# Kernel optimization log

Measured on AMD Instinct MI355X. Metric: run time of the kernel, lower is better.

Reference implementation:

```python
import jax, jax.numpy as jnp
import numpy as np
import math

B, S, D, H = 4, 1024, 1024, 16
DK = D // H


def setup_inputs() -> dict:
    key = jax.random.key(0)
    ks = jax.random.split(key, 12)
    inp = {
        "q": jax.random.normal(ks[0], (B, S, D), jnp.float32),
        "k": jax.random.normal(ks[1], (B, S, D), jnp.float32),
        "v": jax.random.normal(ks[2], (B, S, D), jnp.float32),
        # causal mask, broadcast over batch (0 = masked)
        "mask": jnp.broadcast_to(jnp.tril(jnp.ones((S, S), jnp.int32)), (B, S, S)),
    }
    sc = 1.0 / math.sqrt(D)
    # torch nn.Linear convention: y = x @ W.T + b, W:[out,in]
    inp["Wq"] = jax.random.normal(ks[3], (D, D), jnp.float32) * sc
    inp["bq"] = jnp.zeros((D,), jnp.float32)
    inp["Wk"] = jax.random.normal(ks[4], (D, D), jnp.float32) * sc
    inp["bk"] = jnp.zeros((D,), jnp.float32)
    inp["Wv"] = jax.random.normal(ks[5], (D, D), jnp.float32) * sc
    inp["bv"] = jnp.zeros((D,), jnp.float32)
    inp["Wo"] = jax.random.normal(ks[6], (D, D), jnp.float32) * sc
    inp["bo"] = jnp.zeros((D,), jnp.float32)
    return inp


def _mha(q, k, v, mask, Wq, bq, Wk, bk, Wv, bv, Wo, bo):
    def split_heads(x):  # [B,S,D] -> [B,H,S,DK]
        return x.reshape(B, S, H, DK).transpose(0, 2, 1, 3)

    qh = split_heads(q @ Wq.T + bq)
    kh = split_heads(k @ Wk.T + bk)
    vh = split_heads(v @ Wv.T + bv)

    scores = jnp.einsum("bhqd,bhkd->bhqk", qh, kh) / math.sqrt(DK)
    scores = jnp.where(mask[:, None, :, :] == 0, jnp.float32(-1e9), scores)
    weights = jax.nn.softmax(scores, axis=-1)  # dropout in eval mode -> identity
    out = jnp.einsum("bhqk,bhkd->bhqd", weights, vh)
    out = out.transpose(0, 2, 1, 3).reshape(B, S, D)
    return out @ Wo.T + bo


def reference(q, k, v, mask, Wq, bq, Wk, bk, Wv, bv, Wo, bo):
    return _mha(q, k, v, mask, Wq, bq, Wk, bk, Wv, bv, Wo, bo)
```

## Files before the change

### kernel.cpp

```cpp
#include <hip/hip_runtime.h>

typedef unsigned short u16;
typedef __bf16 bf16x8 __attribute__((ext_vector_type(8)));
typedef float floatx4 __attribute__((ext_vector_type(4)));

#define BB 4
#define SS 1024
#define DD 1024
#define HH 16
#define DKK 64
#define MM (BB*SS)

__device__ __forceinline__ u16 f2bf(float f) {
    union { float f; unsigned int u; } v; v.f = f;
    unsigned int r = v.u + 0x7fffu + ((v.u >> 16) & 1u);
    return (u16)(r >> 16);
}

__device__ __forceinline__ void async16(const u16* g, u16* l) {
    __builtin_amdgcn_global_load_lds(
        (const __attribute__((address_space(1))) void*)g,
        (__attribute__((address_space(3))) void*)l,
        16, 0, 0);
}

__global__ __launch_bounds__(256) void convert_kernel(
    const float* __restrict__ q, const float* __restrict__ k, const float* __restrict__ v,
    const float* __restrict__ Wq, const float* __restrict__ Wk, const float* __restrict__ Wv,
    const float* __restrict__ Wo,
    u16* qb, u16* kb, u16* vb, u16* Wqb, u16* Wkb, u16* Wvb, u16* Wob) {
    const int Q4 = (BB*SS*DD) / 4;
    const int W4 = (DD*DD) / 4;
    int idx = blockIdx.x * 256 + threadIdx.x;
    const float* src; u16* dst; int off;
    if (idx < Q4)            { src = q; dst = qb; off = idx; }
    else if (idx < 2*Q4)     { src = k; dst = kb; off = idx - Q4; }
    else if (idx < 3*Q4)     { src = v; dst = vb; off = idx - 2*Q4; }
    else {
        int r = idx - 3*Q4;
        int wsel = r / W4; off = r - wsel*W4;
        src = wsel==0 ? Wq : wsel==1 ? Wk : wsel==2 ? Wv : Wo;
        dst = wsel==0 ? Wqb : wsel==1 ? Wkb : wsel==2 ? Wvb : Wob;
    }
    float4 x = ((const float4*)src)[off];
    ushort4 y;
    y.x = f2bf(x.x); y.y = f2bf(x.y); y.z = f2bf(x.z); y.w = f2bf(x.w);
    ((ushort4*)dst)[off] = y;
}

__global__ __launch_bounds__(256) void qkv_gemm(
    const u16* __restrict__ qb, const u16* __restrict__ kb, const u16* __restrict__ vb,
    const u16* __restrict__ Wqb, const u16* __restrict__ Wkb, const u16* __restrict__ Wvb,
    const float* __restrict__ bq, const float* __restrict__ bk, const float* __restrict__ bv,
    u16* Qh, u16* Kh, u16* Vt) {
    const int K = DD;
    __shared__ u16 sA[128*32];
    __shared__ u16 sW[128*32];
    int nb = blockIdx.x;
    int m0 = blockIdx.y * 128;
    int which = nb >> 3;
    int n0 = (nb & 7) * 128;
    const u16* A   = which==0 ? qb  : which==1 ? kb  : vb;
    const u16* W   = which==0 ? Wqb : which==1 ? Wkb : Wvb;
    const float* bias = which==0 ? bq : which==1 ? bk : bv;
    u16* Out = which==0 ? Qh : which==1 ? Kh : Vt;
    float scale = which==0 ? 0.125f : 1.0f;

    int t = threadIdx.x;
    int w = t >> 6, l = t & 63, g = l >> 4, c = l & 15;
    int wm = w & 1, wn = w >> 1;
    int sw = (g ^ (c & 3)) * 8;

    floatx4 acc[4][4] = {};

    int srow = t >> 2;
    int sseg = (t & 3) ^ (srow & 3);
    const u16* gA0 = A + (size_t)(m0 + srow) * K + sseg*8;
    const u16* gW0 = W + (size_t)(n0 + srow) * K + sseg*8;
    u16* lA = &sA[t*8];
    u16* lW = &sW[t*8];

    for (int kk = 0; kk < K; kk += 32) {
        __syncthreads();
        async16(gA0 + kk,          lA);
        async16(gA0 + 64*K + kk,   lA + 64*32);
        async16(gW0 + kk,          lW);
        async16(gW0 + 64*K + kk,   lW + 64*32);
        __syncthreads();
        bf16x8 af[4], bf_[4];
        #pragma unroll
        for (int i = 0; i < 4; i++) af[i]  = *(const bf16x8*)&sA[(wm*64 + i*16 + c)*32 + sw];
        #pragma unroll
        for (int j = 0; j < 4; j++) bf_[j] = *(const bf16x8*)&sW[(wn*64 + j*16 + c)*32 + sw];
        #pragma unroll
        for (int i = 0; i < 4; i++)
            #pragma unroll
            for (int j = 0; j < 4; j++)
                acc[i][j] = __builtin_amdgcn_mfma_f32_16x16x32_bf16(af[i], bf_[j], acc[i][j], 0, 0, 0);
    }

    #pragma unroll
    for (int j = 0; j < 4; j++) {
        int col = n0 + wn*64 + j*16 + c;
        float bb = bias[col];
        int h = col >> 6, dk = col & 63;
        #pragma unroll
        for (int i = 0; i < 4; i++) {
            #pragma unroll
            for (int r = 0; r < 4; r++) {
                int row = m0 + wm*64 + i*16 + g*4 + r;
                int b = row >> 10, s = row & 1023;
                float vv = (acc[i][j][r] + bb) * scale;
                u16 bits = f2bf(vv);
                if (which == 2) {
                    Out[((size_t)((b*HH + h)*DKK + dk))*SS + s] = bits;
                } else {
                    Out[((size_t)(b*HH + h)*SS + s)*DKK + dk] = bits;
                }
            }
        }
    }
}

__global__ __launch_bounds__(256) void attn_kernel(
    const u16* __restrict__ Qh, const u16* __restrict__ Kh, const u16* __restrict__ Vt,
    u16* __restrict__ attnO) {
    __shared__ u16 sQ[64*72];
    __shared__ u16 sK[64*72];
    __shared__ u16 sVt[64*72];
    __shared__ u16 sP[64*72];

    int bh = blockIdx.y;
    const u16* Qp  = Qh + (size_t)bh * SS * DKK;
    const u16* Kp  = Kh + (size_t)bh * SS * DKK;
    const u16* Vtp = Vt + (size_t)bh * DKK * SS;
    int b = bh >> 4, h = bh & 15;

    int t = threadIdx.x, w = t >> 6, l = t & 63, g = l >> 4, c = l & 15;
    int wq = w * 16;

    #pragma unroll
    for (int phase = 0; phase < 2; phase++) {
        int qt = phase == 0 ? (15 - (int)blockIdx.x) : (int)blockIdx.x;
        int q0 = qt * 64;

        __syncthreads();
        #pragma unroll
        for (int p = 0; p < 2; p++) {
            int seg = t + p*256;
            int row = seg >> 3, sc = seg & 7;
            *(uint4*)&sQ[row*72 + sc*8] = *(const uint4*)&Qp[(q0 + row)*DKK + sc*8];
        }

        float l_[4] = {0.f, 0.f, 0.f, 0.f};
        floatx4 o[4] = {};

        for (int k0 = 0; k0 <= q0; k0 += 64) {
            __syncthreads();
            #pragma unroll
            for (int p = 0; p < 2; p++) {
                int seg = t + p*256;
                int row = seg >> 3, sc = seg & 7;
                *(uint4*)&sK[row*72 + sc*8]  = *(const uint4*)&Kp[(k0 + row)*DKK + sc*8];
                *(uint4*)&sVt[row*72 + sc*8] = *(const uint4*)&Vtp[row*SS + k0 + sc*8];
            }
            __syncthreads();

            floatx4 sc_[4] = {};
            #pragma unroll
            for (int ks = 0; ks < 2; ks++) {
                bf16x8 aq = *(const bf16x8*)&sQ[(wq + c)*72 + ks*32 + g*8];
                #pragma unroll
                for (int nt = 0; nt < 4; nt++) {
                    bf16x8 bk_ = *(const bf16x8*)&sK[(nt*16 + c)*72 + ks*32 + g*8];
                    sc_[nt] = __builtin_amdgcn_mfma_f32_16x16x32_bf16(aq, bk_, sc_[nt], 0, 0, 0);
                }
            }

            if (k0 == q0) {
                #pragma unroll
                for (int nt = 0; nt < 4; nt++)
                    #pragma unroll
                    for (int r = 0; r < 4; r++) {
                        int qg = wq + g*4 + r;
                        int kg = nt*16 + c;
                        if (kg > qg) sc_[nt][r] = -1e30f;
                    }
            }

            #pragma unroll
            for (int r = 0; r < 4; r++) {
                float rs = 0.f;
                #pragma unroll
                for (int nt = 0; nt < 4; nt++) {
                    float p = __expf(sc_[nt][r]);
                    sc_[nt][r] = p;
                    rs += p;
                }
                rs += __shfl_xor(rs, 1);
                rs += __shfl_xor(rs, 2);
                rs += __shfl_xor(rs, 4);
                rs += __shfl_xor(rs, 8);
                l_[r] += rs;
                int prow = (wq + g*4 + r)*72;
                #pragma unroll
                for (int nt = 0; nt < 4; nt++)
                    sP[prow + nt*16 + c] = f2bf(sc_[nt][r]);
            }

            #pragma unroll
            for (int ks = 0; ks < 2; ks++) {
                bf16x8 ap = *(const bf16x8*)&sP[(wq + c)*72 + ks*32 + g*8];
                #pragma unroll
                for (int nt = 0; nt < 4; nt++) {
                    bf16x8 bv_ = *(const bf16x8*)&sVt[(nt*16 + c)*72 + ks*32 + g*8];
                    o[nt] = __builtin_amdgcn_mfma_f32_16x16x32_bf16(ap, bv_, o[nt], 0, 0, 0);
                }
            }
        }

        #pragma unroll
        for (int r = 0; r < 4; r++) {
            float inv = 1.0f / l_[r];
            int row = q0 + wq + g*4 + r;
            #pragma unroll
            for (int nt = 0; nt < 4; nt++) {
                int dcol = h*64 + nt*16 + c;
                attnO[((size_t)b*SS + row)*DD + dcol] = f2bf(o[nt][r] * inv);
            }
        }
    }
}

__global__ __launch_bounds__(256) void out_gemm(
    const u16* __restrict__ A, const u16* __restrict__ W,
    const float* __restrict__ bo, float* __restrict__ out) {
    const int K = DD;
    __shared__ u16 sA[64*32];
    __shared__ u16 sW[128*32];
    int n0 = blockIdx.x * 128;
    int m0 = blockIdx.y * 64;

    int t = threadIdx.x;
    int w = t >> 6, l = t & 63, g = l >> 4, c = l & 15;
    int wm = w & 1, wn = w >> 1;
    int sw = (g ^ (c & 3)) * 8;

    floatx4 acc[2][4] = {};

    int srow = t >> 2;
    int sseg = (t & 3) ^ (srow & 3);
    const u16* gA0 = A + (size_t)(m0 + srow) * K + sseg*8;
    const u16* gW0 = W + (size_t)(n0 + srow) * K + sseg*8;
    u16* lA = &sA[t*8];
    u16* lW = &sW[t*8];

    for (int kk = 0; kk < K; kk += 32) {
        __syncthreads();
        async16(gA0 + kk,        lA);
        async16(gW0 + kk,        lW);
        async16(gW0 + 64*K + kk, lW + 64*32);
        __syncthreads();
        bf16x8 af[2], bf_[4];
        #pragma unroll
        for (int i = 0; i < 2; i++) af[i]  = *(const bf16x8*)&sA[(wm*32 + i*16 + c)*32 + sw];
        #pragma unroll
        for (int j = 0; j < 4; j++) bf_[j] = *(const bf16x8*)&sW[(wn*64 + j*16 + c)*32 + sw];
        #pragma unroll
        for (int i = 0; i < 2; i++)
            #pragma unroll
            for (int j = 0; j < 4; j++)
                acc[i][j] = __builtin_amdgcn_mfma_f32_16x16x32_bf16(af[i], bf_[j], acc[i][j], 0, 0, 0);
    }

    #pragma unroll
    for (int j = 0; j < 4; j++) {
        int col = n0 + wn*64 + j*16 + c;
        float bb = bo[col];
        #pragma unroll
        for (int i = 0; i < 2; i++) {
            #pragma unroll
            for (int r = 0; r < 4; r++) {
                int row = m0 + wm*32 + i*16 + g*4 + r;
                out[(size_t)row*DD + col] = acc[i][j][r] + bb;
            }
        }
    }
}

extern "C" void kernel_launch(void* const* d_in, const int* in_sizes, int n_in,
                              void* d_out, int out_size, void* d_ws, size_t ws_size,
                              hipStream_t stream) {
    const float* q    = (const float*)d_in[0];
    const float* k    = (const float*)d_in[1];
    const float* v    = (const float*)d_in[2];
    const float* Wq   = (const float*)d_in[4];
    const float* bq   = (const float*)d_in[5];
    const float* Wk   = (const float*)d_in[6];
    const float* bk   = (const float*)d_in[7];
    const float* Wv   = (const float*)d_in[8];
    const float* bv   = (const float*)d_in[9];
    const float* Wo   = (const float*)d_in[10];
    const float* bo   = (const float*)d_in[11];
    float* out = (float*)d_out;

    char* ws = (char*)d_ws;
    const size_t MB = 1024*1024;
    u16* qb   = (u16*)(ws + 0*MB);
    u16* kb   = (u16*)(ws + 8*MB);
    u16* vb   = (u16*)(ws + 16*MB);
    u16* Wqb  = (u16*)(ws + 24*MB);
    u16* Wkb  = (u16*)(ws + 26*MB);
    u16* Wvb  = (u16*)(ws + 28*MB);
    u16* Wob  = (u16*)(ws + 30*MB);
    u16* Qh   = (u16*)(ws + 32*MB);
    u16* Kh   = (u16*)(ws + 40*MB);
    u16* Vt   = (u16*)(ws + 48*MB);
    u16* attn = (u16*)(ws + 56*MB);

    convert_kernel<<<16384, 256, 0, stream>>>(q, k, v, Wq, Wk, Wv, Wo,
                                              qb, kb, vb, Wqb, Wkb, Wvb, Wob);
    qkv_gemm<<<dim3(24, 32), 256, 0, stream>>>(qb, kb, vb, Wqb, Wkb, Wvb,
                                               bq, bk, bv, Qh, Kh, Vt);
    attn_kernel<<<dim3(8, 64), 256, 0, stream>>>(Qh, Kh, Vt, attn);
    out_gemm<<<dim3(8, 64), 256, 0, stream>>>(attn, Wob, bo, out);
}
```

Measured before the change: 226.5 us.

## Double-buffer K/V tiles with async global-to-LDS loads and XOR swizzle

The attention kernel now fetches Q, K and V^T tiles with direct global-to-LDS async loads into double-buffered shared arrays. The next key block is prefetched while the current one is being computed, which drops one barrier per iteration. The padded 72-element row stride is replaced by an XOR swizzle on 16-byte chunks to avoid LDS bank conflicts without padding. Correctness relies on the remaining barrier waiting for the async loads to finish, and the extra buffers use more LDS, which may reduce occupancy.

```diff
diff --git a/kernel.cpp b/kernel.cpp
--- a/kernel.cpp
+++ b/kernel.cpp
@@ -125,9 +125,9 @@
 __global__ __launch_bounds__(256) void attn_kernel(
     const u16* __restrict__ Qh, const u16* __restrict__ Kh, const u16* __restrict__ Vt,
     u16* __restrict__ attnO) {
-    __shared__ u16 sQ[64*72];
-    __shared__ u16 sK[64*72];
-    __shared__ u16 sVt[64*72];
+    __shared__ u16 sQ[64*64];
+    __shared__ u16 sK[2][64*64];
+    __shared__ u16 sVt[2][64*64];
     __shared__ u16 sP[64*72];
 
     int bh = blockIdx.y;
@@ -138,6 +138,11 @@
 
     int t = threadIdx.x, w = t >> 6, l = t & 63, g = l >> 4, c = l & 15;
     int wq = w * 16;
+    int cx = c & 7;
+
+    int qi0 = t, qi1 = t + 256;
+    int r0 = qi0 >> 3, s0 = (qi0 & 7) ^ (r0 & 7);
+    int r1 = qi1 >> 3, s1 = (qi1 & 7) ^ (r1 & 7);
 
     #pragma unroll
     for (int phase = 0; phase < 2; phase++) {
@@ -145,34 +150,35 @@
         int q0 = qt * 64;
 
         __syncthreads();
-        #pragma unroll
-        for (int p = 0; p < 2; p++) {
-            int seg = t + p*256;
-            int row = seg >> 3, sc = seg & 7;
-            *(uint4*)&sQ[row*72 + sc*8] = *(const uint4*)&Qp[(q0 + row)*DKK + sc*8];
-        }
+        async16(&Qp[(q0 + r0)*DKK + s0*8], &sQ[qi0*8]);
+        async16(&Qp[(q0 + r1)*DKK + s1*8], &sQ[qi1*8]);
+        async16(&Kp[(r0)*DKK + s0*8],      &sK[0][qi0*8]);
+        async16(&Kp[(r1)*DKK + s1*8],      &sK[0][qi1*8]);
+        async16(&Vtp[r0*SS + s0*8],        &sVt[0][qi0*8]);
+        async16(&Vtp[r1*SS + s1*8],        &sVt[0][qi1*8]);
 
         float l_[4] = {0.f, 0.f, 0.f, 0.f};
         floatx4 o[4] = {};
+        int cur = 0;
 
         for (int k0 = 0; k0 <= q0; k0 += 64) {
             __syncthreads();
-            #pragma unroll
-            for (int p = 0; p < 2; p++) {
-                int seg = t + p*256;
-                int row = seg >> 3, sc = seg & 7;
-                *(uint4*)&sK[row*72 + sc*8]  = *(const uint4*)&Kp[(k0 + row)*DKK + sc*8];
-                *(uint4*)&sVt[row*72 + sc*8] = *(const uint4*)&Vtp[row*SS + k0 + sc*8];
-            }
-            __syncthreads();
+            int kn = k0 + 64;
+            if (kn <= q0) {
+                async16(&Kp[(kn + r0)*DKK + s0*8], &sK[cur^1][qi0*8]);
+                async16(&Kp[(kn + r1)*DKK + s1*8], &sK[cur^1][qi1*8]);
+                async16(&Vtp[r0*SS + kn + s0*8],   &sVt[cur^1][qi0*8]);
+                async16(&Vtp[r1*SS + kn + s1*8],   &sVt[cur^1][qi1*8]);
+            }
 
             floatx4 sc_[4] = {};
             #pragma unroll
             for (int ks = 0; ks < 2; ks++) {
-                bf16x8 aq = *(const bf16x8*)&sQ[(wq + c)*72 + ks*32 + g*8];
+                int so = ((ks*4 + g) ^ cx) * 8;
+                bf16x8 aq = *(const bf16x8*)&sQ[(wq + c)*64 + so];
                 #pragma unroll
                 for (int nt = 0; nt < 4; nt++) {
-                    bf16x8 bk_ = *(const bf16x8*)&sK[(nt*16 + c)*72 + ks*32 + g*8];
+                    bf16x8 bk_ = *(const bf16x8*)&sK[cur][(nt*16 + c)*64 + so];
                     sc_[nt] = __builtin_amdgcn_mfma_f32_16x16x32_bf16(aq, bk_, sc_[nt], 0, 0, 0);
                 }
             }
@@ -210,13 +216,15 @@
 
             #pragma unroll
             for (int ks = 0; ks < 2; ks++) {
+                int so = ((ks*4 + g) ^ cx) * 8;
                 bf16x8 ap = *(const bf16x8*)&sP[(wq + c)*72 + ks*32 + g*8];
                 #pragma unroll
                 for (int nt = 0; nt < 4; nt++) {
-                    bf16x8 bv_ = *(const bf16x8*)&sVt[(nt*16 + c)*72 + ks*32 + g*8];
+                    bf16x8 bv_ = *(const bf16x8*)&sVt[cur][(nt*16 + c)*64 + so];
                     o[nt] = __builtin_amdgcn_mfma_f32_16x16x32_bf16(ap, bv_, o[nt], 0, 0, 0);
                 }
             }
+            cur ^= 1;
         }
 
         #pragma unroll
```

New measurement: 225.2 us. No clear change (-0.6%).
